# Kernel optimization log

Measured on AMD Instinct MI355X. Metric: run time of the kernel, lower is better.

## Reference

```python
import jax, jax.numpy as jnp
import numpy as np
from jax import lax

NUM_LAYERS = 1000
DIM = 10
BATCH = 2_000_000


def setup_inputs() -> dict:
    key = jax.random.key(0)
    kx, kw, kb = jax.random.split(key, 3)
    x = jax.random.normal(kx, (BATCH, DIM), dtype=jnp.float32)
    # torch Linear weight is [out, in]; stack all 1000 layers: [L, out, in]
    # std = 1/sqrt(DIM) keeps activation scale roughly stable across 1000 layers
    Ws = jax.random.normal(kw, (NUM_LAYERS, DIM, DIM), dtype=jnp.float32) * (DIM ** -0.5)
    bs = jax.random.normal(kb, (NUM_LAYERS, DIM), dtype=jnp.float32) * 0.01
    return {"x": x, "Ws": Ws, "bs": bs}


def reference(x, Ws, bs):
    # Sequential of 1000 Linear(10,10): h <- h @ W_l.T + b_l, no activation.
    def step(h, wb):
        W, b = wb  # W: [out, in], b: [out]
        return h @ W.T + b, None
    out, _ = lax.scan(step, x, (Ws, bs))
    return out
```

## Files before the change

### kernel.cpp

```cpp
#include <hip/hip_runtime.h>

#define NUM_LAYERS 1000
#define DIM 10
#define STRIDE 112
#define LPB 16
#define NBLK 63

__device__ inline void compose_one(const float* __restrict__ src,
                                   float* __restrict__ dst,
                                   int c, int lane) {
    const float* F = src + (size_t)(2 * c) * STRIDE;
    const float* G = src + (size_t)(2 * c + 1) * STRIDE;
    float colf[DIM], o[DIM];
    #pragma unroll
    for (int r = 0; r < DIM; ++r) colf[r] = F[lane * DIM + r];
    #pragma unroll
    for (int r = 0; r < DIM; ++r) {
        float acc = (lane == DIM) ? G[100 + r] : 0.f;
        #pragma unroll
        for (int k = 0; k < DIM; ++k)
            acc += G[k * DIM + r] * colf[k];
        o[r] = acc;
    }
    float* D = dst + (size_t)c * STRIDE;
    #pragma unroll
    for (int r = 0; r < DIM; ++r) D[lane * DIM + r] = o[r];
}

__global__ __launch_bounds__(1024) void compose16(const float* __restrict__ Ws,
                                                  const float* __restrict__ bs,
                                                  float* __restrict__ wsout) {
    __shared__ float A[LPB * STRIDE];
    __shared__ float B[(LPB / 2) * STRIDE];
    const int tid = threadIdx.x;
    const int blk = blockIdx.x;

    for (int e = tid; e < LPB * 100; e += 1024) {
        int ll = e / 100, rem = e % 100;
        int r = rem / 10, k = rem % 10;
        int l = blk * LPB + ll;
        float v = (l < NUM_LAYERS) ? Ws[(size_t)l * 100 + rem]
                                   : (r == k ? 1.f : 0.f);
        A[ll * STRIDE + k * DIM + r] = v;
    }
    for (int e = tid; e < LPB * DIM; e += 1024) {
        int ll = e / DIM, r = e % DIM;
        int l = blk * LPB + ll;
        float v = (l < NUM_LAYERS) ? bs[(size_t)l * DIM + r] : 0.f;
        A[ll * STRIDE + 100 + r] = v;
    }

    const int wave = tid >> 6, lane = tid & 63;
    const float* src = A;
    float* dst = B;
    for (int n = LPB / 2; n >= 1; n >>= 1) {
        __syncthreads();
        if (wave < n && lane <= DIM) compose_one(src, dst, wave, lane);
        const float* t = dst; dst = (float*)src; src = t;
    }
    __syncthreads();
    if (tid < 110) wsout[(size_t)blk * STRIDE + tid] = A[tid];
}

__global__ __launch_bounds__(1024) void compose_tree64(const float* __restrict__ wsin,
                                                       float* __restrict__ aff) {
    __shared__ float A[64 * STRIDE];
    __shared__ float B[32 * STRIDE];
    const int tid = threadIdx.x;

    for (int e = tid; e < 64 * STRIDE; e += 1024) {
        int chunk = e / STRIDE, pos = e % STRIDE;
        float v;
        if (pos >= 110)      v = 0.f;
        else if (chunk < NBLK) v = wsin[(size_t)chunk * STRIDE + pos];
        else v = (pos < 100 && (pos / 10 == pos % 10)) ? 1.f : 0.f;
        A[e] = v;
    }

    const int wave = tid >> 6, lane = tid & 63;
    const float* src = A;
    float* dst = B;
    for (int n = 32; n >= 1; n >>= 1) {
        __syncthreads();
        if (lane <= DIM)
            for (int c = wave; c < n; c += 16)
                compose_one(src, dst, c, lane);
        const float* t = dst; dst = (float*)src; src = t;
    }
    __syncthreads();
    if (tid < 110) {
        if (tid < 100) {
            int j = tid / DIM, r = tid % DIM;
            aff[r * DIM + j] = A[tid];
        } else {
            aff[tid] = A[tid];
        }
    }
}

__global__ __launch_bounds__(256) void apply_affine(const float* __restrict__ x,
                                                    const float* __restrict__ aff,
                                                    float* __restrict__ out,
                                                    int npairs) {
    __shared__ float s[112];
    if (threadIdx.x < 112)
        s[threadIdx.x] = (threadIdx.x < 110) ? aff[threadIdx.x] : 0.f;
    __syncthreads();

    const int t = blockIdx.x * blockDim.x + threadIdx.x;
    if (t >= npairs) return;

    const float4* xin = (const float4*)x + (size_t)t * 5;
    float4 v0 = xin[0], v1 = xin[1], v2 = xin[2], v3 = xin[3], v4 = xin[4];
    float xv[20] = {v0.x, v0.y, v0.z, v0.w,  v1.x, v1.y, v1.z, v1.w,
                    v2.x, v2.y, v2.z, v2.w,  v3.x, v3.y, v3.z, v3.w,
                    v4.x, v4.y, v4.z, v4.w};
    float o[20];
    #pragma unroll
    for (int rr = 0; rr < 2; ++rr) {
        #pragma unroll
        for (int j = 0; j < DIM; ++j) {
            float acc = s[100 + j];
            #pragma unroll
            for (int k = 0; k < DIM; ++k)
                acc += s[j * DIM + k] * xv[rr * DIM + k];
            o[rr * DIM + j] = acc;
        }
    }

    float4* op = (float4*)out + (size_t)t * 5;
    op[0] = make_float4(o[0],  o[1],  o[2],  o[3]);
    op[1] = make_float4(o[4],  o[5],  o[6],  o[7]);
    op[2] = make_float4(o[8],  o[9],  o[10], o[11]);
    op[3] = make_float4(o[12], o[13], o[14], o[15]);
    op[4] = make_float4(o[16], o[17], o[18], o[19]);
}

extern "C" void kernel_launch(void* const* d_in, const int* in_sizes, int n_in,
                              void* d_out, int out_size, void* d_ws, size_t ws_size,
                              hipStream_t stream) {
    const float* x  = (const float*)d_in[0];
    const float* Ws = (const float*)d_in[1];
    const float* bs = (const float*)d_in[2];
    float* out = (float*)d_out;

    float* ws_chunks = (float*)d_ws;
    float* ws_aff    = ws_chunks + NBLK * STRIDE;

    const int batch  = in_sizes[0] / DIM;
    const int npairs = batch / 2;

    compose16<<<NBLK, 1024, 0, stream>>>(Ws, bs, ws_chunks);
    compose_tree64<<<1, 1024, 0, stream>>>(ws_chunks, ws_aff);

    const int threads = 256;
    const int blocks  = (npairs + threads - 1) / threads;
    apply_affine<<<blocks, threads, 0, stream>>>(x, ws_aff, out, npairs);
}
```

Measured before the change: 171.1 us.

## Fuse compose kernels via last-block counter and stage apply I/O through LDS

The two composition kernels are merged into one. The last block to finish, detected with an atomic counter, performs the final tree reduction, which removes one kernel launch at the cost of an extra memset. The apply kernel now loads x into shared memory with coalesced float4 accesses, computes from there, and writes results back through shared memory. This replaces the strided per-thread 5-float4 global accesses, at the cost of extra LDS traffic and syncs.

New measurement: 188.1 us. 1.1x slower.

```diff
diff --git a/kernel.cpp b/kernel.cpp
--- a/kernel.cpp
+++ b/kernel.cpp
@@ -5,6 +5,7 @@
 #define STRIDE 112
 #define LPB 16
 #define NBLK 63
+#define TILE_Q4 1280
 
 __device__ inline void compose_one(const float* __restrict__ src,
                                    float* __restrict__ dst,
@@ -27,11 +28,14 @@
     for (int r = 0; r < DIM; ++r) D[lane * DIM + r] = o[r];
 }
 
-__global__ __launch_bounds__(1024) void compose16(const float* __restrict__ Ws,
-                                                  const float* __restrict__ bs,
-                                                  float* __restrict__ wsout) {
-    __shared__ float A[LPB * STRIDE];
-    __shared__ float B[(LPB / 2) * STRIDE];
+__global__ __launch_bounds__(1024) void compose_fused(const float* __restrict__ Ws,
+                                                      const float* __restrict__ bs,
+                                                      float* __restrict__ wsout,
+                                                      float* __restrict__ aff,
+                                                      unsigned int* __restrict__ counter) {
+    __shared__ float A[64 * STRIDE];
+    __shared__ float B[32 * STRIDE];
+    __shared__ unsigned int s_last;
     const int tid = threadIdx.x;
     const int blk = blockIdx.x;
 
@@ -51,41 +55,45 @@
     }
 
     const int wave = tid >> 6, lane = tid & 63;
-    const float* src = A;
-    float* dst = B;
-    for (int n = LPB / 2; n >= 1; n >>= 1) {
-        __syncthreads();
-        if (wave < n && lane <= DIM) compose_one(src, dst, wave, lane);
-        const float* t = dst; dst = (float*)src; src = t;
+    {
+        const float* src = A;
+        float* dst = B;
+        for (int n = LPB / 2; n >= 1; n >>= 1) {
+            __syncthreads();
+            if (wave < n && lane <= DIM) compose_one(src, dst, wave, lane);
+            const float* t = dst; dst = (float*)src; src = t;
+        }
     }
     __syncthreads();
     if (tid < 110) wsout[(size_t)blk * STRIDE + tid] = A[tid];
-}
 
-__global__ __launch_bounds__(1024) void compose_tree64(const float* __restrict__ wsin,
-                                                       float* __restrict__ aff) {
-    __shared__ float A[64 * STRIDE];
-    __shared__ float B[32 * STRIDE];
-    const int tid = threadIdx.x;
+    __threadfence();
+    __syncthreads();
+    if (tid == 0) s_last = atomicAdd(counter, 1u);
+    __syncthreads();
+    if (s_last != NBLK - 1) return;
 
+    __threadfence();
     for (int e = tid; e < 64 * STRIDE; e += 1024) {
         int chunk = e / STRIDE, pos = e % STRIDE;
         float v;
-        if (pos >= 110)      v = 0.f;
-        else if (chunk < NBLK) v = wsin[(size_t)chunk * STRIDE + pos];
+        if (pos >= 110)        v = 0.f;
+        else if (chunk < NBLK) v = __hip_atomic_load(&wsout[(size_t)chunk * STRIDE + pos],
+                                                     __ATOMIC_RELAXED,
+                                                     __HIP_MEMORY_SCOPE_AGENT);
         else v = (pos < 100 && (pos / 10 == pos % 10)) ? 1.f : 0.f;
         A[e] = v;
     }
-
-    const int wave = tid >> 6, lane = tid & 63;
-    const float* src = A;
-    float* dst = B;
-    for (int n = 32; n >= 1; n >>= 1) {
-        __syncthreads();
-        if (lane <= DIM)
-            for (int c = wave; c < n; c += 16)
-                compose_one(src, dst, c, lane);
-        const float* t = dst; dst = (float*)src; src = t;
+    {
+        const float* src = A;
+        float* dst = B;
+        for (int n = 32; n >= 1; n >>= 1) {
+            __syncthreads();
+            if (lane <= DIM)
+                for (int c = wave; c < n; c += 16)
+                    compose_one(src, dst, c, lane);
+            const float* t = dst; dst = (float*)src; src = t;
+        }
     }
     __syncthreads();
     if (tid < 110) {
@@ -101,39 +109,55 @@
 __global__ __launch_bounds__(256) void apply_affine(const float* __restrict__ x,
                                                     const float* __restrict__ aff,
                                                     float* __restrict__ out,
-                                                    int npairs) {
+                                                    int nq4) {
+    __shared__ float4 lds4[TILE_Q4];
     __shared__ float s[112];
-    if (threadIdx.x < 112)
-        s[threadIdx.x] = (threadIdx.x < 110) ? aff[threadIdx.x] : 0.f;
+    const int tid = threadIdx.x;
+    if (tid < 112) s[tid] = (tid < 110) ? aff[tid] : 0.f;
+
+    const int q0 = blockIdx.x * TILE_Q4;
+    const float4* __restrict__ xin = (const float4*)x;
+    float4* __restrict__ op = (float4*)out;
+
+    #pragma unroll
+    for (int i = 0; i < 5; ++i) {
+        int q = q0 + i * 256 + tid;
+        if (q < nq4) lds4[i * 256 + tid] = xin[q];
+    }
     __syncthreads();
 
-    const int t = blockIdx.x * blockDim.x + threadIdx.x;
-    if (t >= npairs) return;
+    if (q0 + 5 * tid + 5 <= nq4) {
+        float xv[20];
+        #pragma unroll
+        for (int i = 0; i < 5; ++i) {
+            float4 v = lds4[5 * tid + i];
+            xv[4 * i + 0] = v.x; xv[4 * i + 1] = v.y;
+            xv[4 * i + 2] = v.z; xv[4 * i + 3] = v.w;
+        }
+        float o[20];
+        #pragma unroll
+        for (int rr = 0; rr < 2; ++rr) {
+            #pragma unroll
+            for (int j = 0; j < DIM; ++j) {
+                float acc = s[100 + j];
+                #pragma unroll
+                for (int k = 0; k < DIM; ++k)
+                    acc += s[j * DIM + k] * xv[rr * DIM + k];
+                o[rr * DIM + j] = acc;
+            }
+        }
+        #pragma unroll
+        for (int i = 0; i < 5; ++i)
+            lds4[5 * tid + i] = make_float4(o[4 * i + 0], o[4 * i + 1],
+                                            o[4 * i + 2], o[4 * i + 3]);
+    }
+    __syncthreads();
 
-    const float4* xin = (const float4*)x + (size_t)t * 5;
-    float4 v0 = xin[0], v1 = xin[1], v2 = xin[2], v3 = xin[3], v4 = xin[4];
-    float xv[20] = {v0.x, v0.y, v0.z, v0.w,  v1.x, v1.y, v1.z, v1.w,
-                    v2.x, v2.y, v2.z, v2.w,  v3.x, v3.y, v3.z, v3.w,
-                    v4.x, v4.y, v4.z, v4.w};
-    float o[20];
     #pragma unroll
-    for (int rr = 0; rr < 2; ++rr) {
-        #pragma unroll
-        for (int j = 0; j < DIM; ++j) {
-            float acc = s[100 + j];
-            #pragma unroll
-            for (int k = 0; k < DIM; ++k)
-                acc += s[j * DIM + k] * xv[rr * DIM + k];
-            o[rr * DIM + j] = acc;
-        }
+    for (int i = 0; i < 5; ++i) {
+        int q = q0 + i * 256 + tid;
+        if (q < nq4) op[q] = lds4[i * 256 + tid];
     }
-
-    float4* op = (float4*)out + (size_t)t * 5;
-    op[0] = make_float4(o[0],  o[1],  o[2],  o[3]);
-    op[1] = make_float4(o[4],  o[5],  o[6],  o[7]);
-    op[2] = make_float4(o[8],  o[9],  o[10], o[11]);
-    op[3] = make_float4(o[12], o[13], o[14], o[15]);
-    op[4] = make_float4(o[16], o[17], o[18], o[19]);
 }
 
 extern "C" void kernel_launch(void* const* d_in, const int* in_sizes, int n_in,
@@ -146,14 +170,13 @@
 
     float* ws_chunks = (float*)d_ws;
     float* ws_aff    = ws_chunks + NBLK * STRIDE;
+    unsigned int* ws_counter = (unsigned int*)(ws_aff + STRIDE);
 
-    const int batch  = in_sizes[0] / DIM;
-    const int npairs = batch / 2;
+    hipMemsetAsync(ws_counter, 0, sizeof(unsigned int), stream);
 
-    compose16<<<NBLK, 1024, 0, stream>>>(Ws, bs, ws_chunks);
-    compose_tree64<<<1, 1024, 0, stream>>>(ws_chunks, ws_aff);
+    compose_fused<<<NBLK, 1024, 0, stream>>>(Ws, bs, ws_chunks, ws_aff, ws_counter);
 
-    const int threads = 256;
-    const int blocks  = (npairs + threads - 1) / threads;
-    apply_affine<<<blocks, threads, 0, stream>>>(x, ws_aff, out, npairs);
+    const int nq4 = in_sizes[0] / 4;
+    const int blocks = (nq4 + TILE_Q4 - 1) / TILE_Q4;
+    apply_affine<<<blocks, 256, 0, stream>>>(x, ws_aff, out, nq4);
 }
```
